# Kernel optimization log

Hardware: AMD Instinct MI355X
Metric: run time of the kernel (lower is better)

The kernel has to match this reference:

```python
import jax, jax.numpy as jnp
import numpy as np

S, B, H, NH = 2048, 1, 2048, 16
HD = H // NH
ROTARY_BASE = 10000.0
MASK_FILL = -10000.0  # gpt2_attention_mask_func fill value


def _rotate_half(x):
    x1, x2 = jnp.split(x, 2, axis=-1)
    return jnp.concatenate((-x2, x1), axis=-1)


def _rotary_cos_sin(seq_len, dim, dtype):
    inv_freq = 1.0 / (ROTARY_BASE ** (jnp.arange(0, dim, 2, dtype=jnp.float32) / dim))
    t = jnp.arange(seq_len, dtype=jnp.float32)
    freqs = t[:, None] * inv_freq[None, :]          # [s, dim/2]
    emb = jnp.concatenate((freqs, freqs), axis=-1)  # [s, dim]
    # shape [s, 1, 1, dim] to broadcast over (batch, heads)
    return jnp.cos(emb)[:, None, None, :].astype(dtype), jnp.sin(emb)[:, None, None, :].astype(dtype)


def setup_inputs() -> dict:
    key = jax.random.key(0)
    k0, k1, k2 = jax.random.split(key, 3)
    hidden_states = jax.random.normal(k0, (S, B, H), dtype=jnp.float32) * 0.02
    # causal mask: True = masked (upper triangle above diagonal)
    attention_mask = jnp.triu(jnp.ones((1, 1, S, S), dtype=bool), k=1)
    w_qkv = jax.random.normal(k1, (3 * H, H), dtype=jnp.float32) * 0.02
    b_qkv = jnp.zeros((3 * H,), dtype=jnp.float32)
    w_dense = jax.random.normal(k2, (H, H), dtype=jnp.float32) * 0.02
    return {"hidden_states": hidden_states, "attention_mask": attention_mask,
            "w_qkv": w_qkv, "b_qkv": b_qkv, "w_dense": w_dense}


def reference(hidden_states, attention_mask, w_qkv, b_qkv, w_dense):
    s, b, h = hidden_states.shape
    # fused QKV projection: [s, b, 3h]
    mixed = jnp.einsum('sbh,oh->sbo', hidden_states, w_qkv) + b_qkv
    mixed = mixed.reshape(s, b, NH, 3 * HD)
    q, k, v = jnp.split(mixed, 3, axis=-1)  # each [s, b, nh, hd]
    # rotary embedding (rotary_pct == 1 -> full head dim)
    cos, sin = _rotary_cos_sin(s, HD, q.dtype)
    q = q * cos + _rotate_half(q) * sin
    k = k * cos + _rotate_half(k) * sin
    # scaled QK^T: [b, nh, sq, sk]
    norm_factor = jnp.asarray(1.0 / np.sqrt(HD), dtype=q.dtype)
    scores = jnp.einsum('sbnd,tbnd->bnst', q, k) * norm_factor
    scores = jnp.where(attention_mask, jnp.asarray(MASK_FILL, scores.dtype), scores)
    probs = jax.nn.softmax(scores.astype(jnp.float32), axis=-1).astype(scores.dtype)
    # PV: [s, b, nh, hd]
    ctx = jnp.einsum('bnst,tbnd->sbnd', probs, v)
    ctx = ctx.reshape(s, b, h)
    # RowParallelLinear with skip_bias_add: bias returned separately (not added)
    out = jnp.einsum('sbh,oh->sbo', ctx, w_dense)
    return out
```

## Files before the change

kernel.cpp:

```cpp
#include <hip/hip_runtime.h>


#define S_LEN 2048
#define NHEAD 16
#define HDIM  128
#define HID   2048
#define H3    6144

typedef short bf16x8 __attribute__((ext_vector_type(8)));
typedef float f32x4  __attribute__((ext_vector_type(4)));

__device__ __forceinline__ float bf2f(ushort u) {
  union { float f; unsigned int i; } v; v.i = ((unsigned int)u) << 16; return v.f;
}
__device__ __forceinline__ ushort f2bf(float f) {
  union { float f; unsigned int i; } v; v.f = f;
  unsigned int r = v.i + 0x7fffu + ((v.i >> 16) & 1u);
  return (ushort)(r >> 16);
}
__device__ __forceinline__ int4 cvt8(const float* p) {
  float4 a = *(const float4*)p, b = *(const float4*)(p + 4);
  union { ushort u[8]; int4 v; } r;
  r.u[0] = f2bf(a.x); r.u[1] = f2bf(a.y); r.u[2] = f2bf(a.z); r.u[3] = f2bf(a.w);
  r.u[4] = f2bf(b.x); r.u[5] = f2bf(b.y); r.u[6] = f2bf(b.z); r.u[7] = f2bf(b.w);
  return r.v;
}

typedef __attribute__((address_space(1))) const unsigned int gu32;
typedef __attribute__((address_space(3))) unsigned int lu32;
__device__ __forceinline__ void async16(const void* g, void* l) {
  __builtin_amdgcn_global_load_lds((gu32*)g, (lu32*)l, 16, 0, 0);
}

__global__ __launch_bounds__(256) void cvt_bf16(const float* __restrict__ src,
                                                ushort* __restrict__ dst, int n8) {
  int i = blockIdx.x * 256 + threadIdx.x;
  if (i < n8) *(int4*)&dst[(size_t)i * 8] = cvt8(&src[(size_t)i * 8]);
}

template<int BM, int BN, bool HAS_BIAS, bool OUT_F32>
__global__ __launch_bounds__(256) void gemm_async(const ushort* __restrict__ A,
                                                  const ushort* __restrict__ W,
                                                  const float* __restrict__ bias,
                                                  void* __restrict__ Cv,
                                                  int N, int K, int AS, int AH) {
  __shared__ __align__(16) ushort As[BM * 64];
  __shared__ __align__(16) ushort Ws[BN * 64];
  const int tid  = threadIdx.x;
  const int lane = tid & 63;
  const int w    = tid >> 6;
  const int wr   = w >> 1, wc = w & 1;
  const int quad = lane >> 4, ln15 = lane & 15;
  const int tm = blockIdx.y * BM, tn = blockIdx.x * BN;
  constexpr int MI = BM / 32, NJ = BN / 32;

  f32x4 acc[MI][NJ];
#pragma unroll
  for (int i = 0; i < MI; ++i)
#pragma unroll
    for (int j = 0; j < NJ; ++j) acc[i][j] = (f32x4){0.f, 0.f, 0.f, 0.f};

  const int lrow8 = lane >> 3;
  const int gsw   = (lane & 7) ^ lrow8;
  const int sw    = ln15 & 7;

  for (int k0 = 0; k0 < K; k0 += 64) {
    for (int r = w; r < (BM + BN) / 8; r += 4) {
      if (r < BM / 8) {
        const int ka = k0 + gsw * 8;
        async16(&A[(size_t)(tm + r * 8 + lrow8) * AS + (ka >> 7) * AH + (ka & 127)],
                &As[r * 8 * 64]);
      } else {
        const int rb = r - BM / 8;
        async16(&W[(size_t)(tn + rb * 8 + lrow8) * K + k0 + gsw * 8],
                &Ws[rb * 8 * 64]);
      }
    }
    __syncthreads();
#pragma unroll
    for (int kk = 0; kk < 2; ++kk) {
      const int slot = ((kk * 4 + quad) ^ sw) * 8;
      bf16x8 af[MI], bw[NJ];
#pragma unroll
      for (int i = 0; i < MI; ++i)
        af[i] = *(const bf16x8*)&As[((BM / 2) * wr + 16 * i + ln15) * 64 + slot];
#pragma unroll
      for (int j = 0; j < NJ; ++j)
        bw[j] = *(const bf16x8*)&Ws[((BN / 2) * wc + 16 * j + ln15) * 64 + slot];
#pragma unroll
      for (int i = 0; i < MI; ++i)
#pragma unroll
        for (int j = 0; j < NJ; ++j)
          acc[i][j] = __builtin_amdgcn_mfma_f32_16x16x32_bf16(af[i], bw[j], acc[i][j], 0, 0, 0);
    }
    __syncthreads();
  }

#pragma unroll
  for (int i = 0; i < MI; ++i)
#pragma unroll
    for (int j = 0; j < NJ; ++j) {
      int col = tn + (BN / 2) * wc + 16 * j + ln15;
      float badd = HAS_BIAS ? bias[col] : 0.0f;
#pragma unroll
      for (int r = 0; r < 4; ++r) {
        int row = tm + (BM / 2) * wr + 16 * i + 4 * quad + r;
        float val = acc[i][j][r] + badd;
        if (OUT_F32) ((float*)Cv)[(size_t)row * N + col] = val;
        else         ((ushort*)Cv)[(size_t)row * N + col] = f2bf(val);
      }
    }
}

template<bool A_F32, bool HAS_BIAS, bool OUT_F32>
__global__ __launch_bounds__(256) void gemm_bt(const void* __restrict__ Av,
                                               const float* __restrict__ W,
                                               const float* __restrict__ bias,
                                               void* __restrict__ Cv,
                                               int M, int N, int K, int AS, int AH) {
  __shared__ __align__(16) ushort As[128 * 40];
  __shared__ __align__(16) ushort Ws[128 * 40];
  const int tid  = threadIdx.x;
  const int lane = tid & 63;
  const int w    = tid >> 6;
  const int wr   = w >> 1, wc = w & 1;
  const int quad = lane >> 4, ln15 = lane & 15;
  const int tm = blockIdx.y * 128, tn = blockIdx.x * 128;

  f32x4 acc[4][4];
#pragma unroll
  for (int i = 0; i < 4; ++i)
#pragma unroll
    for (int j = 0; j < 4; ++j) acc[i][j] = (f32x4){0.f, 0.f, 0.f, 0.f};

  const int row0 = tid >> 2, row1 = row0 + 64;
  const int kp   = (tid & 3) * 8;

  for (int k0 = 0; k0 < K; k0 += 32) {
    const int ka   = k0 + kp;
    const int aoff = (ka >> 7) * AH + (ka & 127);
    if (A_F32) {
      const float* A = (const float*)Av;
      *(int4*)&As[row0 * 40 + kp] = cvt8(&A[(size_t)(tm + row0) * AS + aoff]);
      *(int4*)&As[row1 * 40 + kp] = cvt8(&A[(size_t)(tm + row1) * AS + aoff]);
    } else {
      const ushort* A = (const ushort*)Av;
      *(int4*)&As[row0 * 40 + kp] = *(const int4*)&A[(size_t)(tm + row0) * AS + aoff];
      *(int4*)&As[row1 * 40 + kp] = *(const int4*)&A[(size_t)(tm + row1) * AS + aoff];
    }
    *(int4*)&Ws[row0 * 40 + kp] = cvt8(&W[(size_t)(tn + row0) * K + ka]);
    *(int4*)&Ws[row1 * 40 + kp] = cvt8(&W[(size_t)(tn + row1) * K + ka]);
    __syncthreads();
    bf16x8 af[4], bw[4];
#pragma unroll
    for (int i = 0; i < 4; ++i)
      af[i] = *(const bf16x8*)&As[(64 * wr + 16 * i + ln15) * 40 + quad * 8];
#pragma unroll
    for (int j = 0; j < 4; ++j)
      bw[j] = *(const bf16x8*)&Ws[(64 * wc + 16 * j + ln15) * 40 + quad * 8];
#pragma unroll
    for (int i = 0; i < 4; ++i)
#pragma unroll
      for (int j = 0; j < 4; ++j)
        acc[i][j] = __builtin_amdgcn_mfma_f32_16x16x32_bf16(af[i], bw[j], acc[i][j], 0, 0, 0);
    __syncthreads();
  }

#pragma unroll
  for (int i = 0; i < 4; ++i)
#pragma unroll
    for (int j = 0; j < 4; ++j) {
      int col = tn + 64 * wc + 16 * j + ln15;
      float badd = HAS_BIAS ? bias[col] : 0.0f;
#pragma unroll
      for (int r = 0; r < 4; ++r) {
        int row = tm + 64 * wr + 16 * i + 4 * quad + r;
        float val = acc[i][j][r] + badd;
        if (OUT_F32) ((float*)Cv)[(size_t)row * N + col] = val;
        else         ((ushort*)Cv)[(size_t)row * N + col] = f2bf(val);
      }
    }
}

__global__ __launch_bounds__(256) void rope_kernel(ushort* __restrict__ mixed) {
  int t = blockIdx.x * 256 + threadIdx.x;
  int d = t & 63;
  int n = (t >> 6) & (NHEAD - 1);
  int s = t >> 10;
  ushort* base = mixed + (size_t)s * H3 + n * 384;
  float invf = exp2f((float)d * (-13.287712379549449f / 64.0f));
  float ang = (float)s * invf;
  float si, c; sincosf(ang, &si, &c);
  float q0 = bf2f(base[d]),       q1 = bf2f(base[64 + d]);
  float k0 = bf2f(base[128 + d]), k1 = bf2f(base[192 + d]);
  base[d]       = f2bf(q0 * c - q1 * si);
  base[64 + d]  = f2bf(q1 * c + q0 * si);
  base[128 + d] = f2bf(k0 * c - k1 * si);
  base[192 + d] = f2bf(k1 * c + k0 * si);
}

__global__ __launch_bounds__(256) void v_transpose(const ushort* __restrict__ mixed,
                                                   ushort* __restrict__ vt) {
  __shared__ __align__(16) ushort Vl[64 * 136];
  const int tid = threadIdx.x;
  const int sb = blockIdx.x;
  const int n  = blockIdx.y;
#pragma unroll
  for (int it = 0; it < 4; ++it) {
    int c = tid + it * 256;
    int row = c >> 4, dp = (c & 15) * 8;
    *(int4*)&Vl[row * 136 + dp] =
        *(const int4*)&mixed[(size_t)(sb * 64 + row) * H3 + n * 384 + 256 + dp];
  }
  __syncthreads();
#pragma unroll
  for (int it = 0; it < 4; ++it) {
    int c = tid + it * 256;
    int d = c >> 3, sp = (c & 7) * 8;
    union { ushort u[8]; int4 v; } pk;
#pragma unroll
    for (int e = 0; e < 8; ++e) pk.u[e] = Vl[(sp + e) * 136 + d];
    *(int4*)&vt[((size_t)(n * 128 + d)) * S_LEN + sb * 64 + sp] = pk.v;
  }
}

__global__ __launch_bounds__(256, 3) void attn_kernel(const ushort* __restrict__ mixed,
                                                      const ushort* __restrict__ vt,
                                                      ushort* __restrict__ ctx,
                                                      int CS, int CH) {
  __shared__ __align__(16) ushort Ks[2][64 * 128];
  __shared__ __align__(16) ushort Vs[128 * 64];

  const int tid  = threadIdx.x;
  const int lane = tid & 63;
  const int w    = tid >> 6;
  const int quad = lane >> 4, ln15 = lane & 15;
  const int qb = blockIdx.x;
  const int n  = blockIdx.y;
  const float scale = 0.08838834764831845f;

  const ushort* Kg = mixed + n * 384 + 128;
  const ushort* Vg = vt + (size_t)n * 128 * S_LEN;

  bf16x8 aqr[4];
#pragma unroll
  for (int ks = 0; ks < 4; ++ks)
    aqr[ks] = *(const bf16x8*)&mixed[(size_t)(qb * 64 + 16 * w + ln15) * H3 + n * 384
                                     + ks * 32 + quad * 8];

  f32x4 acc_o[8];
#pragma unroll
  for (int jt = 0; jt < 8; ++jt) acc_o[jt] = (f32x4){0.f, 0.f, 0.f, 0.f};
  float m_run = -1e30f, l_run = 0.0f;

  const int krow = lane >> 4, kcs = lane & 15;
  const int vrow = lane >> 3, vcs = lane & 7;
  const int swz  = ln15 & 7;

#define STAGE_K(KT, BUF)                                                        \
  { _Pragma("unroll")                                                           \
    for (int i = 0; i < 4; ++i) {                                               \
      int sig = ((w & 2) << 4) + 8 * i + ((w & 1) << 2) + krow;                 \
      int kcl = kcs ^ ((i * 4 + krow) & 7);                                     \
      async16(&Kg[(size_t)((KT) * 64 + sig) * H3 + kcl * 8],                    \
              &Ks[BUF][(w * 16 + i * 4) * 128]);                                \
    } }
#define STAGE_V(KT)                                                             \
  { _Pragma("unroll")                                                           \
    for (int i = 0; i < 4; ++i) {                                               \
      int vr = w * 32 + i * 8 + vrow;                                           \
      int vcl = vcs ^ (vr & 7);                                                 \
      async16(&Vg[(size_t)vr * S_LEN + (KT) * 64 + vcl * 8],                    \
              &Vs[(w * 32 + i * 8) * 64]);                                      \
    } }

  int cur = 0;
  STAGE_K(0, 0);
  __syncthreads();

  const int ig = qb * 64 + 16 * w + ln15;

  for (int kt = 0; kt <= qb; ++kt) {
    STAGE_V(kt);
    if (kt < qb) STAGE_K(kt + 1, cur ^ 1);

    f32x4 sacc[4];
#pragma unroll
    for (int jt = 0; jt < 4; ++jt) sacc[jt] = (f32x4){0.f, 0.f, 0.f, 0.f};
#pragma unroll
    for (int ks = 0; ks < 4; ++ks) {
#pragma unroll
      for (int jt = 0; jt < 4; ++jt) {
        bf16x8 bk = *(const bf16x8*)&Ks[cur][(16 * jt + ln15) * 128
                                            + ((ks * 4 + quad) ^ swz) * 8];
        sacc[jt] = __builtin_amdgcn_mfma_f32_16x16x32_bf16(bk, aqr[ks], sacc[jt], 0, 0, 0);
      }
    }

    float sv[4][4];
#pragma unroll
    for (int jt = 0; jt < 4; ++jt) {
#pragma unroll
      for (int r = 0; r < 4; ++r) {
        int kl = ((jt & 2) << 4) + 8 * quad + ((jt & 1) << 2) + r;
        int jg = kt * 64 + kl;
        float x = sacc[jt][r] * scale;
        sv[jt][r] = (jg > ig) ? -10000.0f : x;
      }
    }

    float tmx = sv[0][0];
#pragma unroll
    for (int jt = 0; jt < 4; ++jt)
#pragma unroll
      for (int r = 0; r < 4; ++r) tmx = fmaxf(tmx, sv[jt][r]);
    tmx = fmaxf(tmx, __shfl_xor(tmx, 16));
    tmx = fmaxf(tmx, __shfl_xor(tmx, 32));

    float m_new = fmaxf(m_run, tmx);
    float alpha = __expf(m_run - m_new);
    m_run = m_new;

    float p[4][4];
    float ps = 0.0f;
#pragma unroll
    for (int jt = 0; jt < 4; ++jt)
#pragma unroll
      for (int r = 0; r < 4; ++r) {
        p[jt][r] = __expf(sv[jt][r] - m_run);
        ps += p[jt][r];
      }
    ps += __shfl_xor(ps, 16);
    ps += __shfl_xor(ps, 32);
    l_run = alpha * l_run + ps;

    float aw[4];
#pragma unroll
    for (int r = 0; r < 4; ++r) aw[r] = __shfl(alpha, 4 * quad + r);
#pragma unroll
    for (int jt = 0; jt < 8; ++jt)
#pragma unroll
      for (int r = 0; r < 4; ++r) acc_o[jt][r] *= aw[r];

    bf16x8 ap0, ap1;
#pragma unroll
    for (int j = 0; j < 4; ++j) {
      ap0[j]     = (short)f2bf(p[0][j]);
      ap0[4 + j] = (short)f2bf(p[1][j]);
      ap1[j]     = (short)f2bf(p[2][j]);
      ap1[4 + j] = (short)f2bf(p[3][j]);
    }

    __syncthreads();

#pragma unroll
    for (int jt = 0; jt < 8; ++jt) {
      bf16x8 bv0 = *(const bf16x8*)&Vs[(16 * jt + ln15) * 64 + ((quad) ^ swz) * 8];
      acc_o[jt] = __builtin_amdgcn_mfma_f32_16x16x32_bf16(ap0, bv0, acc_o[jt], 0, 0, 0);
      bf16x8 bv1 = *(const bf16x8*)&Vs[(16 * jt + ln15) * 64 + ((4 + quad) ^ swz) * 8];
      acc_o[jt] = __builtin_amdgcn_mfma_f32_16x16x32_bf16(ap1, bv1, acc_o[jt], 0, 0, 0);
    }

    __syncthreads();
    cur ^= 1;
  }
#undef STAGE_K
#undef STAGE_V

  float rinv[4];
#pragma unroll
  for (int r = 0; r < 4; ++r) rinv[r] = 1.0f / __shfl(l_run, 4 * quad + r);
#pragma unroll
  for (int jt = 0; jt < 8; ++jt)
#pragma unroll
    for (int r = 0; r < 4; ++r) {
      int row = qb * 64 + 16 * w + 4 * quad + r;
      int col = 16 * jt + ln15;
      ctx[(size_t)row * CS + n * CH + col] = f2bf(acc_o[jt][r] * rinv[r]);
    }
}

extern "C" void kernel_launch(void* const* d_in, const int* in_sizes, int n_in,
                              void* d_out, int out_size, void* d_ws, size_t ws_size,
                              hipStream_t stream) {
  const float* hidden  = (const float*)d_in[0];
  const float* w_qkv   = (const float*)d_in[2];
  const float* b_qkv   = (const float*)d_in[3];
  const float* w_dense = (const float*)d_in[4];
  float* out = (float*)d_out;

  char* ws = (char*)d_ws;

  const size_t wq_b    = (size_t)H3 * HID * 2;
  const size_t h_b     = (size_t)S_LEN * HID * 2;
  const size_t mixed_b = (size_t)S_LEN * H3 * 2;
  const size_t vt_b    = (size_t)NHEAD * HDIM * S_LEN * 2;
  const size_t fast_need = wq_b + h_b + mixed_b + vt_b;

  if (ws_size >= fast_need) {
    ushort* WQ    = (ushort*)ws;
    ushort* Hbf   = (ushort*)(ws + wq_b);
    ushort* mixed = (ushort*)(ws + wq_b + h_b);
    ushort* vt    = (ushort*)(ws + wq_b + h_b + mixed_b);
    ushort* WD    = WQ;
    ushort* ctx   = mixed;

    cvt_bf16<<<2048, 256, 0, stream>>>(hidden, Hbf, S_LEN * HID / 8);
    cvt_bf16<<<6144, 256, 0, stream>>>(w_qkv, WQ, H3 * HID / 8);
    gemm_async<128, 128, true, false><<<dim3(48, 16), 256, 0, stream>>>(
        Hbf, WQ, b_qkv, mixed, H3, HID, HID, 128);
    rope_kernel<<<8192, 256, 0, stream>>>(mixed);
    v_transpose<<<dim3(32, 16), 256, 0, stream>>>(mixed, vt);
    attn_kernel<<<dim3(32, 16), 256, 0, stream>>>(mixed, vt, ctx, H3, 384);
    cvt_bf16<<<2048, 256, 0, stream>>>(w_dense, WD, HID * HID / 8);
    gemm_async<64, 128, false, true><<<dim3(16, 32), 256, 0, stream>>>(
        ctx, WD, nullptr, out, HID, HID, H3, 384);
  } else {
    ushort* mixed = (ushort*)ws;
    ushort* vt    = (ushort*)(ws + mixed_b);
    const bool big = ws_size >= mixed_b + vt_b + (size_t)S_LEN * HID * 2;
    ushort* ctx = big ? (ushort*)(ws + mixed_b + vt_b) : mixed;
    const int CS = big ? HID  : H3;
    const int CH = big ? HDIM : 384;

    gemm_bt<true, true, false><<<dim3(48, 16), 256, 0, stream>>>(
        hidden, w_qkv, b_qkv, mixed, S_LEN, H3, HID, HID, HDIM);
    rope_kernel<<<8192, 256, 0, stream>>>(mixed);
    v_transpose<<<dim3(32, 16), 256, 0, stream>>>(mixed, vt);
    attn_kernel<<<dim3(32, 16), 256, 0, stream>>>(mixed, vt, ctx, CS, CH);
    gemm_bt<false, false, true><<<dim3(16, 16), 256, 0, stream>>>(
        ctx, w_dense, nullptr, out, S_LEN, HID, HID, CS, CH);
  }
}
```

Measured before the change: 300.6 us.

## Split long causal attention query blocks across two KV halves with merge kernel

```diff
diff --git a/kernel.cpp b/kernel.cpp
--- a/kernel.cpp
+++ b/kernel.cpp
@@ -227,7 +227,8 @@
 __global__ __launch_bounds__(256, 3) void attn_kernel(const ushort* __restrict__ mixed,
                                                       const ushort* __restrict__ vt,
                                                       ushort* __restrict__ ctx,
-                                                      int CS, int CH) {
+                                                      int CS, int CH,
+                                                      float* __restrict__ part) {
   __shared__ __align__(16) ushort Ks[2][64 * 128];
   __shared__ __align__(16) ushort Vs[128 * 64];
 
@@ -235,9 +236,15 @@
   const int lane = tid & 63;
   const int w    = tid >> 6;
   const int quad = lane >> 4, ln15 = lane & 15;
-  const int qb = blockIdx.x;
+  const int p  = blockIdx.x;
   const int n  = blockIdx.y;
   const float scale = 0.08838834764831845f;
+
+  int qb, kt0, kt1, pslot;
+  if (part == nullptr) { qb = p;      kt0 = 0;             kt1 = qb + 1;        pslot = -1; }
+  else if (p < 16)     { qb = p;      kt0 = 0;             kt1 = qb + 1;        pslot = -1; }
+  else if (p < 32)     { qb = 47 - p; kt0 = 0;             kt1 = (qb + 1) >> 1; pslot = (n * 16 + qb - 16) * 2; }
+  else                 { qb = 63 - p; kt0 = (qb + 1) >> 1; kt1 = qb + 1;        pslot = (n * 16 + qb - 16) * 2 + 1; }
 
   const ushort* Kg = mixed + n * 384 + 128;
   const ushort* Vg = vt + (size_t)n * 128 * S_LEN;
@@ -275,14 +282,14 @@
     } }
 
   int cur = 0;
-  STAGE_K(0, 0);
+  STAGE_K(kt0, 0);
   __syncthreads();
 
   const int ig = qb * 64 + 16 * w + ln15;
 
-  for (int kt = 0; kt <= qb; ++kt) {
+  for (int kt = kt0; kt < kt1; ++kt) {
     STAGE_V(kt);
-    if (kt < qb) STAGE_K(kt + 1, cur ^ 1);
+    if (kt + 1 < kt1) STAGE_K(kt + 1, cur ^ 1);
 
     f32x4 sacc[4];
 #pragma unroll
@@ -321,14 +328,14 @@
     float alpha = __expf(m_run - m_new);
     m_run = m_new;
 
-    float p[4][4];
+    float pv[4][4];
     float ps = 0.0f;
 #pragma unroll
     for (int jt = 0; jt < 4; ++jt)
 #pragma unroll
       for (int r = 0; r < 4; ++r) {
-        p[jt][r] = __expf(sv[jt][r] - m_run);
-        ps += p[jt][r];
+        pv[jt][r] = __expf(sv[jt][r] - m_run);
+        ps += pv[jt][r];
       }
     ps += __shfl_xor(ps, 16);
     ps += __shfl_xor(ps, 32);
@@ -345,10 +352,10 @@
     bf16x8 ap0, ap1;
 #pragma unroll
     for (int j = 0; j < 4; ++j) {
-      ap0[j]     = (short)f2bf(p[0][j]);
-      ap0[4 + j] = (short)f2bf(p[1][j]);
-      ap1[j]     = (short)f2bf(p[2][j]);
-      ap1[4 + j] = (short)f2bf(p[3][j]);
+      ap0[j]     = (short)f2bf(pv[0][j]);
+      ap0[4 + j] = (short)f2bf(pv[1][j]);
+      ap1[j]     = (short)f2bf(pv[2][j]);
+      ap1[4 + j] = (short)f2bf(pv[3][j]);
     }
 
     __syncthreads();
@@ -367,17 +374,59 @@
 #undef STAGE_K
 #undef STAGE_V
 
-  float rinv[4];
-#pragma unroll
-  for (int r = 0; r < 4; ++r) rinv[r] = 1.0f / __shfl(l_run, 4 * quad + r);
-#pragma unroll
-  for (int jt = 0; jt < 8; ++jt)
-#pragma unroll
-    for (int r = 0; r < 4; ++r) {
-      int row = qb * 64 + 16 * w + 4 * quad + r;
-      int col = 16 * jt + ln15;
-      ctx[(size_t)row * CS + n * CH + col] = f2bf(acc_o[jt][r] * rinv[r]);
-    }
+  if (pslot < 0) {
+    float rinv[4];
+#pragma unroll
+    for (int r = 0; r < 4; ++r) rinv[r] = 1.0f / __shfl(l_run, 4 * quad + r);
+#pragma unroll
+    for (int jt = 0; jt < 8; ++jt)
+#pragma unroll
+      for (int r = 0; r < 4; ++r) {
+        int row = qb * 64 + 16 * w + 4 * quad + r;
+        int col = 16 * jt + ln15;
+        ctx[(size_t)row * CS + n * CH + col] = f2bf(acc_o[jt][r] * rinv[r]);
+      }
+  } else {
+    float* pp = part + (size_t)pslot * 8320;
+#pragma unroll
+    for (int jt = 0; jt < 8; ++jt)
+#pragma unroll
+      for (int r = 0; r < 4; ++r)
+        pp[(16 * w + 4 * quad + r) * 128 + 16 * jt + ln15] = acc_o[jt][r];
+    if (quad == 0) {
+      pp[8192 + 16 * w + ln15] = m_run;
+      pp[8256 + 16 * w + ln15] = l_run;
+    }
+  }
+}
+
+__global__ __launch_bounds__(256) void merge_kernel(const float* __restrict__ part,
+                                                    ushort* __restrict__ ctx,
+                                                    int CS, int CH) {
+  const int xqb = blockIdx.x, n = blockIdx.y;
+  const int qb = 16 + xqb;
+  const float* pA = part + (size_t)((n * 16 + xqb) * 2 + 0) * 8320;
+  const float* pB = part + (size_t)((n * 16 + xqb) * 2 + 1) * 8320;
+  const int row = threadIdx.x >> 2;
+  const int c0  = (threadIdx.x & 3) * 32;
+  float mA = pA[8192 + row], mB = pB[8192 + row];
+  float lA = pA[8256 + row], lB = pB[8256 + row];
+  float m  = fmaxf(mA, mB);
+  float wA = __expf(mA - m), wB = __expf(mB - m);
+  float rl = 1.0f / (wA * lA + wB * lB);
+  wA *= rl; wB *= rl;
+  ushort* dst = ctx + (size_t)(qb * 64 + row) * CS + n * CH + c0;
+#pragma unroll
+  for (int j = 0; j < 32; j += 4) {
+    float4 a = *(const float4*)&pA[row * 128 + c0 + j];
+    float4 b = *(const float4*)&pB[row * 128 + c0 + j];
+    ushort4 o;
+    o.x = f2bf(wA * a.x + wB * b.x);
+    o.y = f2bf(wA * a.y + wB * b.y);
+    o.z = f2bf(wA * a.z + wB * b.z);
+    o.w = f2bf(wA * a.w + wB * b.w);
+    *(ushort4*)&dst[j] = o;
+  }
 }
 
 extern "C" void kernel_launch(void* const* d_in, const int* in_sizes, int n_in,
@@ -404,6 +453,7 @@
     ushort* vt    = (ushort*)(ws + wq_b + h_b + mixed_b);
     ushort* WD    = WQ;
     ushort* ctx   = mixed;
+    float* partb  = (float*)ws;
 
     cvt_bf16<<<2048, 256, 0, stream>>>(hidden, Hbf, S_LEN * HID / 8);
     cvt_bf16<<<6144, 256, 0, stream>>>(w_qkv, WQ, H3 * HID / 8);
@@ -411,7 +461,8 @@
         Hbf, WQ, b_qkv, mixed, H3, HID, HID, 128);
     rope_kernel<<<8192, 256, 0, stream>>>(mixed);
     v_transpose<<<dim3(32, 16), 256, 0, stream>>>(mixed, vt);
-    attn_kernel<<<dim3(32, 16), 256, 0, stream>>>(mixed, vt, ctx, H3, 384);
+    attn_kernel<<<dim3(48, 16), 256, 0, stream>>>(mixed, vt, ctx, H3, 384, partb);
+    merge_kernel<<<dim3(16, 16), 256, 0, stream>>>(partb, ctx, H3, 384);
     cvt_bf16<<<2048, 256, 0, stream>>>(w_dense, WD, HID * HID / 8);
     gemm_async<64, 128, false, true><<<dim3(16, 32), 256, 0, stream>>>(
         ctx, WD, nullptr, out, HID, HID, H3, 384);
@@ -427,7 +478,7 @@
         hidden, w_qkv, b_qkv, mixed, S_LEN, H3, HID, HID, HDIM);
     rope_kernel<<<8192, 256, 0, stream>>>(mixed);
     v_transpose<<<dim3(32, 16), 256, 0, stream>>>(mixed, vt);
-    attn_kernel<<<dim3(32, 16), 256, 0, stream>>>(mixed, vt, ctx, CS, CH);
+    attn_kernel<<<dim3(32, 16), 256, 0, stream>>>(mixed, vt, ctx, CS, CH, nullptr);
     gemm_bt<false, false, true><<<dim3(16, 16), 256, 0, stream>>>(
         ctx, w_dense, nullptr, out, S_LEN, HID, HID, CS, CH);
   }
```

Measured after the change: 284.5 us. 1.06x faster.
